# Kernel tuning notes

Hardware: AMD Instinct MI355X
Metric: run time of the kernel (lower is better)

Reference implementation:

```python
import jax, jax.numpy as jnp
import numpy as np
from jax import lax

EPS = 1e-8

def squash(x, axis=-1):
    # s = (|x|^2 / (1+|x|^2)) * x / |x|, norm over `axis`
    sq = jnp.sum(x * x, axis=axis, keepdims=True)
    return (sq / (1.0 + sq)) * x / jnp.sqrt(sq + EPS)

def _conv(x, w, b, stride):
    y = lax.conv_general_dilated(x, w, window_strides=(stride, stride), padding='VALID',
                                 dimension_numbers=('NCHW', 'OIHW', 'NCHW'))
    return y + b[None, :, None, None]

def setup_inputs() -> dict:
    key = jax.random.key(0)
    ks = jax.random.split(key, 12)
    B = 256
    return {
        'x': jax.random.uniform(ks[0], (B, 1, 28, 28), jnp.float32),
        'conv1_w': jax.random.normal(ks[1], (256, 1, 9, 9), jnp.float32) * 0.1,
        'conv1_b': jax.random.normal(ks[2], (256,), jnp.float32) * 0.01,
        'conv2_w': jax.random.normal(ks[3], (256, 256, 9, 9), jnp.float32) * 0.02,
        'conv2_b': jax.random.normal(ks[4], (256,), jnp.float32) * 0.01,
        'W': jax.random.normal(ks[5], (10, 1152, 8, 16), jnp.float32) * 0.05,
        'dec_w1': jax.random.normal(ks[6], (160, 512), jnp.float32) * 0.05,
        'dec_b1': jnp.zeros((512,), jnp.float32),
        'dec_w2': jax.random.normal(ks[7], (512, 1024), jnp.float32) * 0.04,
        'dec_b2': jnp.zeros((1024,), jnp.float32),
        'dec_w3': jax.random.normal(ks[8], (1024, 784), jnp.float32) * 0.03,
        'dec_b3': jnp.zeros((784,), jnp.float32),
    }

def reference(x, conv1_w, conv1_b, conv2_w, conv2_b, W, dec_w1, dec_b1, dec_w2, dec_b2, dec_w3, dec_b3):
    B = x.shape[0]
    h = jax.nn.relu(_conv(x, conv1_w, conv1_b, 1))          # [B,256,20,20]
    h = jax.nn.relu(_conv(h, conv2_w, conv2_b, 2))          # [B,256,6,6]
    u = squash(h.reshape(B, 1152, 8))                       # [B,1152,8]
    # u_hat[b,c,n,f] = sum_d u[b,n,d] * W[c,n,d,f]
    u_hat = jnp.einsum('bnd,cndf->bcnf', u, W)              # [B,10,1152,16]
    # dynamic routing, 3 iterations; softmax over the 1152 input-capsule axis
    # (faithful to original: softmax dim=2, b constant along the 16 axis)
    b_logits = jnp.zeros((B, 10, 1152), u_hat.dtype)
    v = None
    for i in range(3):
        c = jax.nn.softmax(b_logits, axis=2)                # [B,10,1152]
        s = jnp.einsum('bcn,bcnf->bcf', c, u_hat)           # [B,10,16]
        v = squash(s)
        if i != 2:
            b_logits = b_logits + jnp.einsum('bcf,bcnf->bcn', v, u_hat)
    class_probs = jnp.sqrt(jnp.sum(v * v, axis=-1) + EPS)   # [B,10]
    idx = jnp.argmax(class_probs, axis=-1)
    mask = jax.nn.one_hot(idx, 10, dtype=v.dtype)           # [B,10]
    r = (v * mask[:, :, None]).reshape(B, 160)
    r = jax.nn.relu(r @ dec_w1 + dec_b1)
    r = jax.nn.relu(r @ dec_w2 + dec_b2)
    recons = jax.nn.sigmoid(r @ dec_w3 + dec_b3)            # [B,784]
    return (class_probs, recons)
```

## Files before the change

kernel.cpp:

```cpp
#include <hip/hip_runtime.h>
#include <hip/hip_bf16.h>
#include <math.h>

typedef _Float16 f16;
typedef f16 f16x8 __attribute__((ext_vector_type(8)));
typedef f16 f16x4 __attribute__((ext_vector_type(4)));
typedef float f32x16 __attribute__((ext_vector_type(16)));


__global__ __launch_bounds__(256) void conv1_kernel(
    const float* __restrict__ x, const float* __restrict__ w,
    const float* __restrict__ bias, f16* __restrict__ outh,
    float* __restrict__ outf, int mode)
{
    const int b = blockIdx.y;
    const int cg = blockIdx.x;
    const int t = threadIdx.x;

    __shared__ float xs[784];
    __shared__ float wt[81 * 16];
    __shared__ float bs[16];

    for (int i = t; i < 784; i += 256) xs[i] = x[b * 784 + i];
    for (int i = t; i < 1296; i += 256) {
        int k = i >> 4, cc = i & 15;
        wt[i] = w[(cg * 16 + cc) * 81 + k];
    }
    if (t < 16) bs[t] = bias[cg * 16 + t];
    __syncthreads();

    if (t >= 200) return;
    const int pos = t * 2;
    const int oy = pos / 20, ox = pos % 20;
    float4 A0[4], A1[4];
    #pragma unroll
    for (int g = 0; g < 4; ++g) { A0[g] = make_float4(0,0,0,0); A1[g] = make_float4(0,0,0,0); }

    for (int ky = 0; ky < 9; ++ky) {
        const float* xr = &xs[(oy + ky) * 28 + ox];
        #pragma unroll
        for (int kx = 0; kx < 9; ++kx) {
            float x0 = xr[kx], x1 = xr[kx + 1];
            const float4* wp = (const float4*)&wt[(ky * 9 + kx) << 4];
            #pragma unroll
            for (int g = 0; g < 4; ++g) {
                float4 wv = wp[g];
                A0[g].x = fmaf(x0, wv.x, A0[g].x); A0[g].y = fmaf(x0, wv.y, A0[g].y);
                A0[g].z = fmaf(x0, wv.z, A0[g].z); A0[g].w = fmaf(x0, wv.w, A0[g].w);
                A1[g].x = fmaf(x1, wv.x, A1[g].x); A1[g].y = fmaf(x1, wv.y, A1[g].y);
                A1[g].z = fmaf(x1, wv.z, A1[g].z); A1[g].w = fmaf(x1, wv.w, A1[g].w);
            }
        }
    }

    float va[16], vb[16];
    #pragma unroll
    for (int g = 0; g < 4; ++g) {
        va[g*4+0] = fmaxf(A0[g].x + bs[g*4+0], 0.f);
        va[g*4+1] = fmaxf(A0[g].y + bs[g*4+1], 0.f);
        va[g*4+2] = fmaxf(A0[g].z + bs[g*4+2], 0.f);
        va[g*4+3] = fmaxf(A0[g].w + bs[g*4+3], 0.f);
        vb[g*4+0] = fmaxf(A1[g].x + bs[g*4+0], 0.f);
        vb[g*4+1] = fmaxf(A1[g].y + bs[g*4+1], 0.f);
        vb[g*4+2] = fmaxf(A1[g].z + bs[g*4+2], 0.f);
        vb[g*4+3] = fmaxf(A1[g].w + bs[g*4+3], 0.f);
    }

    if (mode == 0) {
        size_t base0 = ((size_t)b * 400 + pos) * 256 + cg * 16;
        f16x8 H;
        #pragma unroll
        for (int q = 0; q < 8; ++q) H[q] = (f16)va[q];
        *(f16x8*)(outh + base0) = H;
        #pragma unroll
        for (int q = 0; q < 8; ++q) H[q] = (f16)va[8+q];
        *(f16x8*)(outh + base0 + 8) = H;
        size_t base1 = base0 + 256;
        #pragma unroll
        for (int q = 0; q < 8; ++q) H[q] = (f16)vb[q];
        *(f16x8*)(outh + base1) = H;
        #pragma unroll
        for (int q = 0; q < 8; ++q) H[q] = (f16)vb[8+q];
        *(f16x8*)(outh + base1 + 8) = H;
    } else {
        #pragma unroll
        for (int q = 0; q < 16; ++q) {
            size_t base = (size_t)(b * 256 + cg * 16 + q) * 400 + pos;
            outf[base] = va[q]; outf[base + 1] = vb[q];
        }
    }
}

__global__ __launch_bounds__(256) void wprep_kernel(
    const float* __restrict__ w, f16* __restrict__ Wf)
{
    const int co = blockIdx.x, t = threadIdx.x;
    __shared__ float wl[20736];
    for (int i = t; i < 20736; i += 256) wl[i] = w[(size_t)co * 20736 + i];
    __syncthreads();
    for (int tap = 0; tap < 81; ++tap) {
        size_t o = ((size_t)tap * 256 + co) * 256 + t;
        Wf[o] = (f16)wl[t * 81 + tap];
    }
}

__global__ __launch_bounds__(256) void wprep2_kernel(
    const float* __restrict__ W, f16* __restrict__ Wr)
{
    const int i = blockIdx.x * 256 + threadIdx.x;
    Wr[i] = (f16)W[i];
}

struct C2R { f16x8 a0, a1, b0, b1, b2, b3; };

#define C2_LOADSET(R, gstep) do { \
    const int tap_ = (gstep) >> 3; \
    const int kc_ = ((gstep) & 7) << 5; \
    const int ky_ = tap_ / 9, kx_ = tap_ - ky_ * 9; \
    const int ao_ = (ky_ * 20 + kx_) * 256 + kc_; \
    const int bo_ = tap_ * 65536 + kc_; \
    R.a0 = *(const f16x8*)(A + paRow + ao_ + sl0 * 8); \
    R.a1 = *(const f16x8*)(A + paRow + ao_ + sl1 * 8); \
    R.b0 = *(const f16x8*)(B + pbRow + bo_); \
    R.b1 = *(const f16x8*)(B + pbRow + bo_ + 8); \
    R.b2 = *(const f16x8*)(B + pbRow + bo_ + 16); \
    R.b3 = *(const f16x8*)(B + pbRow + bo_ + 24); \
} while (0)

#define C2_STORESET(BB, R) do { \
    *(f16x8*)((char*)sA[BB] + wbA0) = R.a0; \
    *(f16x8*)((char*)sA[BB] + wbA1) = R.a1; \
    *(f16x8*)((char*)sB[BB] + wbB)          = R.b0; \
    *(f16x8*)((char*)sB[BB] + wbB + 4096)   = R.b1; \
    *(f16x8*)((char*)sB[BB] + wbB + 8192)   = R.b2; \
    *(f16x8*)((char*)sB[BB] + wbB + 12288)  = R.b3; \
} while (0)

#define C2_COMPUTE(BB) do { \
    _Pragma("unroll") \
    for (int h = 0; h < 2; ++h) { \
        f16x8 a0 = *(const f16x8*)((char*)sA[BB] + offA[h]); \
        f16x8 a1 = *(const f16x8*)((char*)sA[BB] + offA[h] + 512); \
        f16x8 b0 = *(const f16x8*)((char*)sB[BB] + offB[h]); \
        f16x8 b1 = *(const f16x8*)((char*)sB[BB] + offB[h] + 512); \
        f16x8 b2 = *(const f16x8*)((char*)sB[BB] + offB[h] + 1024); \
        f16x8 b3 = *(const f16x8*)((char*)sB[BB] + offB[h] + 1536); \
        acc00 = __builtin_amdgcn_mfma_f32_32x32x16_f16(a0, b0, acc00, 0, 0, 0); \
        acc01 = __builtin_amdgcn_mfma_f32_32x32x16_f16(a0, b1, acc01, 0, 0, 0); \
        acc02 = __builtin_amdgcn_mfma_f32_32x32x16_f16(a0, b2, acc02, 0, 0, 0); \
        acc03 = __builtin_amdgcn_mfma_f32_32x32x16_f16(a0, b3, acc03, 0, 0, 0); \
        acc10 = __builtin_amdgcn_mfma_f32_32x32x16_f16(a1, b0, acc10, 0, 0, 0); \
        acc11 = __builtin_amdgcn_mfma_f32_32x32x16_f16(a1, b1, acc11, 0, 0, 0); \
        acc12 = __builtin_amdgcn_mfma_f32_32x32x16_f16(a1, b2, acc12, 0, 0, 0); \
        acc13 = __builtin_amdgcn_mfma_f32_32x32x16_f16(a1, b3, acc13, 0, 0, 0); \
    } \
} while (0)

#define C2_BAR() do { \
    asm volatile("s_waitcnt lgkmcnt(0)" ::: "memory"); \
    __builtin_amdgcn_s_barrier(); \
    asm volatile("" ::: "memory"); \
} while (0)

__global__ __launch_bounds__(256, 2) void conv2_f16(
    const f16* __restrict__ A, const f16* __restrict__ B,
    float* __restrict__ partial, int nslice, int spk, int nwg)
{
    const int cpx = nwg >> 3;
    const int wg = (blockIdx.x & 7) * cpx + (blockIdx.x >> 3);
    const int mblk = wg / nslice;
    const int kslice = wg % nslice;

    const int t = threadIdx.x;
    const int lane = t & 63, wv = t >> 6;
    const int wm = wv >> 1, wn = wv & 1;

    __shared__ f16 sA[2][4096], sB[2][8192];

    const int strow = t >> 1;
    const int sl0 = (t & 1) * 2;
    const int sl1 = sl0 + 1;
    const int m0 = mblk * 128 + strow;
    const int b0_ = m0 / 36, s0_ = m0 % 36;
    const int paRow = b0_ * 102400 + ((s0_ / 6) * 40 + (s0_ % 6) * 2) * 256;
    const int pbRow = t * 256;

    const int wbA0 = sl0 * 2048 + strow * 16;
    const int wbA1 = sl1 * 2048 + strow * 16;
    const int wbB  = t * 16;

    const int kh = lane >> 5;
    const int rArow = wm * 64 + (lane & 31);
    const int rBrow = wn * 128 + (lane & 31);
    int offA[2], offB[2];
    #pragma unroll
    for (int h = 0; h < 2; ++h) {
        offA[h] = ((h * 2 + kh) << 11) + rArow * 16;
        offB[h] = ((h * 2 + kh) << 12) + rBrow * 16;
    }

    f32x16 acc00 = {}, acc01 = {}, acc02 = {}, acc03 = {};
    f32x16 acc10 = {}, acc11 = {}, acc12 = {}, acc13 = {};

    const int g0 = kslice * spk;
    C2R r0s, r1s;
    C2_LOADSET(r0s, g0);
    C2_LOADSET(r1s, g0 + 1);

    for (int s = 0; s < spk; s += 2) {
        C2_STORESET(0, r0s);
        C2_BAR();
        if (s + 2 < spk) C2_LOADSET(r0s, g0 + s + 2);
        C2_COMPUTE(0);

        C2_STORESET(1, r1s);
        C2_BAR();
        if (s + 3 < spk) C2_LOADSET(r1s, g0 + s + 3);
        C2_COMPUTE(1);
    }

    float* pp = partial + (size_t)kslice * 2359296;
    const int colb = wn * 128 + (lane & 31);
    const int rowb = mblk * 128 + wm * 64 + 4 * (lane >> 5);
    #pragma unroll
    for (int a = 0; a < 2; ++a) {
        #pragma unroll
        for (int nf = 0; nf < 4; ++nf) {
            const f32x16 v = (a == 0)
                ? (nf == 0 ? acc00 : nf == 1 ? acc01 : nf == 2 ? acc02 : acc03)
                : (nf == 0 ? acc10 : nf == 1 ? acc11 : nf == 2 ? acc12 : acc13);
            const int col = colb + nf * 32;
            const int rb = rowb + a * 32;
            #pragma unroll
            for (int r = 0; r < 16; ++r) {
                int row = rb + (r & 3) + 8 * (r >> 2);
                pp[(size_t)row * 256 + col] = v[r];
            }
        }
    }
}

__global__ __launch_bounds__(256) void reduce_kernel(
    const float* __restrict__ partial, const float* __restrict__ bias,
    float* __restrict__ u, int ks)
{
    const int b = blockIdx.x, t = threadIdx.x;
    __shared__ float ld[36 * 260];
    const int cog = t & 63;
    const int srow = t >> 6;
    const float4 bv = *(const float4*)(bias + cog * 4);
    #pragma unroll
    for (int q = 0; q < 9; ++q) {
        const int s = srow + q * 4;
        const size_t idx = ((size_t)(b * 36 + s)) * 256 + cog * 4;
        float4 a = bv;
        for (int k = 0; k < ks; ++k) {
            float4 p = *(const float4*)(partial + (size_t)k * 2359296 + idx);
            a.x += p.x; a.y += p.y; a.z += p.z; a.w += p.w;
        }
        a.x = fmaxf(a.x, 0.f); a.y = fmaxf(a.y, 0.f);
        a.z = fmaxf(a.z, 0.f); a.w = fmaxf(a.w, 0.f);
        *(float4*)&ld[s * 260 + cog * 4] = a;
    }
    __syncthreads();
    for (int n = t; n < 1152; n += 256) {
        const int f0 = n * 8;
        float vals[8]; float sq = 0.f;
        int co = f0 / 36;
        int s = f0 - co * 36;
        #pragma unroll
        for (int d = 0; d < 8; ++d) {
            float v = ld[s * 260 + co];
            vals[d] = v; sq += v * v;
            if (++s == 36) { s = 0; ++co; }
        }
        float scale = (sq / (1.f + sq)) / sqrtf(sq + 1e-8f);
        #pragma unroll
        for (int d = 0; d < 8; ++d) u[(size_t)b * 9216 + f0 + d] = vals[d] * scale;
    }
}

#define C2_CHUNK 2
__global__ __launch_bounds__(384) void conv2_kernel(
    const float* __restrict__ in, const float* __restrict__ w,
    const float* __restrict__ bias, float* __restrict__ out)
{
    const int bg = blockIdx.y;
    const int ct = blockIdx.x;
    const int t = threadIdx.x;

    __shared__ float wl[C2_CHUNK][81][64];
    __shared__ float il[C2_CHUNK][4][20][24];

    const int cg = t & 15;
    const int slot = t >> 4;
    const int bb = slot / 6;
    const int oy = slot % 6;

    float4 acc[6];
    #pragma unroll
    for (int i = 0; i < 6; ++i) acc[i] = make_float4(0,0,0,0);

    for (int cc0 = 0; cc0 < 256; cc0 += C2_CHUNK) {
        for (int idx = t; idx < C2_CHUNK * 5184; idx += 384) {
            int ci = idx / 5184;
            int r = idx - ci * 5184;
            int kk = r >> 6;
            int co = r & 63;
            wl[ci][kk][co] = w[(size_t)(ct * 64 + co) * 20736 + (cc0 + ci) * 81 + kk];
        }
        for (int idx = t; idx < C2_CHUNK * 1600; idx += 384) {
            int ci = idx / 1600;
            int r = idx - ci * 1600;
            int bb2 = r / 400;
            int p = r - bb2 * 400;
            int y = p / 20;
            int xx = p - y * 20;
            il[ci][bb2][y][(xx & 1) * 12 + (xx >> 1)] =
                in[(size_t)((bg * 4 + bb2) * 256 + cc0 + ci) * 400 + p];
        }
        __syncthreads();

        #pragma unroll
        for (int ci = 0; ci < C2_CHUNK; ++ci) {
            for (int ky = 0; ky < 9; ++ky) {
                const int y = oy * 2 + ky;
                const float4* rowp = (const float4*)&il[ci][bb][y][0];
                float a[24];
                #pragma unroll
                for (int q = 0; q < 6; ++q) *(((float4*)a) + q) = rowp[q];
                #pragma unroll
                for (int kx = 0; kx < 9; ++kx) {
                    const int k = ky * 9 + kx;
                    float4 wv = *(const float4*)&wl[ci][k][cg * 4];
                    const int base = (kx & 1) ? (12 + (kx >> 1)) : (kx >> 1);
                    #pragma unroll
                    for (int ox = 0; ox < 6; ++ox) {
                        float av = a[base + ox];
                        acc[ox].x = fmaf(av, wv.x, acc[ox].x);
                        acc[ox].y = fmaf(av, wv.y, acc[ox].y);
                        acc[ox].z = fmaf(av, wv.z, acc[ox].z);
                        acc[ox].w = fmaf(av, wv.w, acc[ox].w);
                    }
                }
            }
        }
        __syncthreads();
    }

    const int b = bg * 4 + bb;
    const int c0 = ct * 64 + cg * 4;
    float4 bv = *(const float4*)&bias[c0];
    #pragma unroll
    for (int ox = 0; ox < 6; ++ox) {
        int sdx = oy * 6 + ox;
        size_t ob = (size_t)b * 9216 + sdx;
        out[ob + (size_t)(c0 + 0) * 36] = fmaxf(acc[ox].x + bv.x, 0.f);
        out[ob + (size_t)(c0 + 1) * 36] = fmaxf(acc[ox].y + bv.y, 0.f);
        out[ob + (size_t)(c0 + 2) * 36] = fmaxf(acc[ox].z + bv.z, 0.f);
        out[ob + (size_t)(c0 + 3) * 36] = fmaxf(acc[ox].w + bv.w, 0.f);
    }
}

__global__ __launch_bounds__(256) void squash_kernel(float* __restrict__ h)
{
    const int cap = blockIdx.x * 256 + threadIdx.x;
    float4* p = (float4*)(h + (size_t)cap * 8);
    float4 v0 = p[0], v1 = p[1];
    float sq = v0.x*v0.x + v0.y*v0.y + v0.z*v0.z + v0.w*v0.w
             + v1.x*v1.x + v1.y*v1.y + v1.z*v1.z + v1.w*v1.w;
    float scale = (sq / (1.f + sq)) / sqrtf(sq + 1e-8f);
    v0.x *= scale; v0.y *= scale; v0.z *= scale; v0.w *= scale;
    v1.x *= scale; v1.y *= scale; v1.z *= scale; v1.w *= scale;
    p[0] = v0; p[1] = v1;
}

__global__ __launch_bounds__(256) void routing_kernel(
    const float* __restrict__ u, const f16* __restrict__ Wr,
    float* __restrict__ cp_out, float* __restrict__ vbuf)
{
    const int wg = ((blockIdx.x & 7) * 320) + (blockIdx.x >> 3);
    const int c = wg >> 8;
    const int b = wg & 255;
    const int t = threadIdx.x;
    const int lane = t & 63, wid = t >> 6;

    __shared__ float uh[1152 * 16];
    __shared__ float cl[1152];
    __shared__ float red[256];
    __shared__ float rtmp[8];
    __shared__ float vv[16];

    {
        const int fg = t & 3, ng = t >> 2;
        const f16* Wc = Wr + (size_t)c * 147456;
        const float* ub = u + (size_t)b * 9216;
        for (int j = 0; j < 18; ++j) {
            int n = ng + (j << 6);
            const f16* wn = Wc + n * 128 + fg * 4;
            float4 u0 = *(const float4*)(ub + n * 8);
            float4 u1 = *(const float4*)(ub + n * 8 + 4);
            float ud[8] = {u0.x, u0.y, u0.z, u0.w, u1.x, u1.y, u1.z, u1.w};
            float ax = 0.f, ay = 0.f, az = 0.f, aw = 0.f;
            #pragma unroll
            for (int d = 0; d < 8; ++d) {
                f16x4 w4 = *(const f16x4*)(wn + (d << 4));
                ax = fmaf(ud[d], (float)w4[0], ax);
                ay = fmaf(ud[d], (float)w4[1], ay);
                az = fmaf(ud[d], (float)w4[2], az);
                aw = fmaf(ud[d], (float)w4[3], aw);
            }
            *(float4*)&uh[(n << 4) + (fg << 2)] = make_float4(ax, ay, az, aw);
        }
    }
    __syncthreads();

    float blr[5] = {0.f, 0.f, 0.f, 0.f, 0.f};
    const int nown = (t < 128) ? 5 : 4;

    for (int it = 0; it < 3; ++it) {
        float m = -1e30f;
        #pragma unroll
        for (int k = 0; k < 5; ++k) if (k < nown) m = fmaxf(m, blr[k]);
        #pragma unroll
        for (int o = 32; o > 0; o >>= 1) m = fmaxf(m, __shfl_xor(m, o));
        if (lane == 0) rtmp[wid] = m;
        __syncthreads();
        m = fmaxf(fmaxf(rtmp[0], rtmp[1]), fmaxf(rtmp[2], rtmp[3]));

        float sum = 0.f;
        #pragma unroll
        for (int k = 0; k < 5; ++k) if (k < nown) {
            float e = __expf(blr[k] - m);
            cl[t + (k << 8)] = e;
            sum += e;
        }
        #pragma unroll
        for (int o = 32; o > 0; o >>= 1) sum += __shfl_xor(sum, o);
        if (lane == 0) rtmp[4 + wid] = sum;
        __syncthreads();
        float inv = 1.f / (rtmp[4] + rtmp[5] + rtmp[6] + rtmp[7]);

        const int f = t & 15, g = t >> 4;
        float sacc = 0.f;
        for (int n = g; n < 1152; n += 16)
            sacc = fmaf(cl[n], uh[(n << 4) + f], sacc);
        red[(g << 4) + f] = sacc;
        __syncthreads();
        if (t < 16) {
            float sv = 0.f;
            #pragma unroll
            for (int gg = 0; gg < 16; ++gg) sv += red[(gg << 4) + t];
            sv *= inv;
            float sq = sv * sv;
            #pragma unroll
            for (int o = 8; o > 0; o >>= 1) sq += __shfl_xor(sq, o);
            float scale = (sq / (1.f + sq)) / sqrtf(sq + 1e-8f);
            vv[t] = sv * scale;
        }
        __syncthreads();

        if (it < 2) {
            #pragma unroll
            for (int k = 0; k < 5; ++k) if (k < nown) {
                const int n = t + (k << 8);
                const float4* up = (const float4*)&uh[n << 4];
                float4 q0 = up[0], q1 = up[1], q2 = up[2], q3 = up[3];
                blr[k] +=
                    q0.x*vv[0]  + q0.y*vv[1]  + q0.z*vv[2]  + q0.w*vv[3] +
                    q1.x*vv[4]  + q1.y*vv[5]  + q1.z*vv[6]  + q1.w*vv[7] +
                    q2.x*vv[8]  + q2.y*vv[9]  + q2.z*vv[10] + q2.w*vv[11] +
                    q3.x*vv[12] + q3.y*vv[13] + q3.z*vv[14] + q3.w*vv[15];
            }
        }
    }

    if (t < 16) {
        float v_ = vv[t];
        float s2 = v_ * v_;
        #pragma unroll
        for (int o = 8; o > 0; o >>= 1) s2 += __shfl_xor(s2, o);
        if (t == 0) cp_out[b * 10 + c] = sqrtf(s2 + 1e-8f);
        vbuf[((b * 10 + c) << 4) + t] = v_;
    }
}

__global__ __launch_bounds__(256) void dec1_kernel(
    const float* __restrict__ cp, const float* __restrict__ vbuf,
    const float* __restrict__ W1, const float* __restrict__ B1,
    float* __restrict__ h1)
{
    const int b = blockIdx.x, t = threadIdx.x;
    __shared__ float r16[16];

    float best = cp[b * 10];
    int idx = 0;
    #pragma unroll
    for (int cc = 1; cc < 10; ++cc) {
        float p = cp[b * 10 + cc];
        if (p > best) { best = p; idx = cc; }
    }
    if (t < 16) r16[t] = vbuf[(b * 10 + idx) * 16 + t];
    __syncthreads();

    float a0 = B1[t], a1 = B1[t + 256];
    const float* w = W1 + (size_t)idx * 16 * 512 + t;
    #pragma unroll
    for (int k = 0; k < 16; ++k) {
        float rv = r16[k];
        a0 = fmaf(rv, w[k * 512], a0);
        a1 = fmaf(rv, w[k * 512 + 256], a1);
    }
    h1[(size_t)b * 512 + t] = fmaxf(a0, 0.f);
    h1[(size_t)b * 512 + t + 256] = fmaxf(a1, 0.f);
}

__global__ __launch_bounds__(256) void dec2_kernel(
    const float* __restrict__ h1, const float* __restrict__ W2,
    const float* __restrict__ B2, float* __restrict__ h2)
{
    const int ot = blockIdx.x, bt = blockIdx.y, t = threadIdx.x;
    const int bb = bt * 16 + (t >> 4);
    const int o = ot * 128 + (t & 15) * 8;

    float acc[8];
    float4 bv0 = *(const float4*)(B2 + o);
    float4 bv1 = *(const float4*)(B2 + o + 4);
    acc[0]=bv0.x; acc[1]=bv0.y; acc[2]=bv0.z; acc[3]=bv0.w;
    acc[4]=bv1.x; acc[5]=bv1.y; acc[6]=bv1.z; acc[7]=bv1.w;

    const float* hr = h1 + (size_t)bb * 512;
    #pragma unroll 4
    for (int k = 0; k < 512; ++k) {
        float hv = hr[k];
        float4 w0 = *(const float4*)(W2 + (size_t)k * 1024 + o);
        float4 w1 = *(const float4*)(W2 + (size_t)k * 1024 + o + 4);
        acc[0] = fmaf(hv, w0.x, acc[0]); acc[1] = fmaf(hv, w0.y, acc[1]);
        acc[2] = fmaf(hv, w0.z, acc[2]); acc[3] = fmaf(hv, w0.w, acc[3]);
        acc[4] = fmaf(hv, w1.x, acc[4]); acc[5] = fmaf(hv, w1.y, acc[5]);
        acc[6] = fmaf(hv, w1.z, acc[6]); acc[7] = fmaf(hv, w1.w, acc[7]);
    }
    float* hw = h2 + (size_t)bb * 1024 + o;
    #pragma unroll
    for (int q = 0; q < 8; ++q) hw[q] = fmaxf(acc[q], 0.f);
}

__global__ __launch_bounds__(256) void dec3_kernel(
    const float* __restrict__ h2, const float* __restrict__ W3,
    const float* __restrict__ B3, float* __restrict__ out)
{
    const int ot = blockIdx.x, bt = blockIdx.y, t = threadIdx.x;
    const int bb = bt * 16 + (t >> 4);
    const int o = ot * 64 + (t & 15) * 4;
    if (o >= 784) return;

    float4 bv = *(const float4*)(B3 + o);
    float acc[4] = {bv.x, bv.y, bv.z, bv.w};

    const float* hr = h2 + (size_t)bb * 1024;
    #pragma unroll 4
    for (int k = 0; k < 1024; ++k) {
        float hv = hr[k];
        float4 w0 = *(const float4*)(W3 + (size_t)k * 784 + o);
        acc[0] = fmaf(hv, w0.x, acc[0]); acc[1] = fmaf(hv, w0.y, acc[1]);
        acc[2] = fmaf(hv, w0.z, acc[2]); acc[3] = fmaf(hv, w0.w, acc[3]);
    }
    float* ow = out + (size_t)bb * 784 + o;
    #pragma unroll
    for (int q = 0; q < 4; ++q) ow[q] = 1.f / (1.f + expf(-acc[q]));
}

extern "C" void kernel_launch(void* const* d_in, const int* in_sizes, int n_in,
                              void* d_out, int out_size, void* d_ws, size_t ws_size,
                              hipStream_t stream) {
    const float* x   = (const float*)d_in[0];
    const float* w1  = (const float*)d_in[1];
    const float* b1  = (const float*)d_in[2];
    const float* w2  = (const float*)d_in[3];
    const float* b2  = (const float*)d_in[4];
    const float* W   = (const float*)d_in[5];
    const float* dw1 = (const float*)d_in[6];
    const float* db1 = (const float*)d_in[7];
    const float* dw2 = (const float*)d_in[8];
    const float* db2 = (const float*)d_in[9];
    const float* dw3 = (const float*)d_in[10];
    const float* db3 = (const float*)d_in[11];

    float* ws   = (float*)d_ws;
    float* outp = (float*)d_out;

    const size_t avail = ws_size / 4;
    int ks = 0;
    if      (avail >= 16498688ull + 6*2359296ull + 40960ull) ks = 6;
    else if (avail >= 16498688ull + 4*2359296ull + 40960ull) ks = 4;
    else if (avail >= 16498688ull + 2*2359296ull + 40960ull) ks = 2;
    else if (avail >= 16498688ull + 1*2359296ull + 40960ull) ks = 1;

    if (ks > 0) {
        f16* Af = (f16*)ws;
        f16* Wf = (f16*)(ws + 13107200);
        f16* Wr = (f16*)(ws + 15761408);
        float* partial = ws + 16498688;
        float* vbuf = ws + 16498688 + (size_t)ks * 2359296;
        float* u  = ws;
        float* h1 = ws + 13107200;
        float* h2 = ws + 13238272;

        const int nwg = 72 * ks;
        conv1_kernel<<<dim3(16, 256), 256, 0, stream>>>(x, w1, b1, Af, nullptr, 0);
        wprep_kernel<<<256, 256, 0, stream>>>(w2, Wf);
        wprep2_kernel<<<5760, 256, 0, stream>>>(W, Wr);
        conv2_f16<<<nwg, 256, 0, stream>>>(Af, Wf, partial, ks, 648 / ks, nwg);
        reduce_kernel<<<256, 256, 0, stream>>>(partial, b2, u, ks);
        routing_kernel<<<2560, 256, 0, stream>>>(u, Wr, outp, vbuf);
        dec1_kernel<<<256, 256, 0, stream>>>(outp, vbuf, dw1, db1, h1);
        dec2_kernel<<<dim3(8, 16), 256, 0, stream>>>(h1, dw2, db2, h2);
        dec3_kernel<<<dim3(13, 16), 256, 0, stream>>>(h2, dw3, db3, outp + 2560);
    } else {
        float* c1   = ws;
        float* c2   = c1 + 26214400;
        float* vbuf = c2 + 2359296;
        float* h1   = vbuf + 40960;
        float* h2   = h1 + 131072;
        f16* Wr     = (f16*)(h2 + 262144);
        conv1_kernel<<<dim3(16, 256), 256, 0, stream>>>(x, w1, b1, nullptr, c1, 1);
        wprep2_kernel<<<5760, 256, 0, stream>>>(W, Wr);
        conv2_kernel<<<dim3(4, 64), 384, 0, stream>>>(c1, w2, b2, c2);
        squash_kernel<<<1152, 256, 0, stream>>>(c2);
        routing_kernel<<<2560, 256, 0, stream>>>(c2, Wr, outp, vbuf);
        dec1_kernel<<<256, 256, 0, stream>>>(outp, vbuf, dw1, db1, h1);
        dec2_kernel<<<dim3(8, 16), 256, 0, stream>>>(h1, dw2, db2, h2);
        dec3_kernel<<<dim3(13, 16), 256, 0, stream>>>(h2, dw3, db3, outp + 2560);
    }
}
```

Before: 540.1 us.

## Store conv2 split-K partials as f16 transposed and raise split count

The conv2 split-K partial sums are now stored as f16 in a channel-major transposed layout, which halves partial-buffer traffic and lets the reduce kernel read contiguous f16x4 runs per channel. The split count rises to as many as 12 slices, adding more workgroups for better GPU fill, and the launch-bounds occupancy hint goes from 2 to 3. An odd-spk tail is also handled. Rounding partials to f16 before the sum costs some accuracy, and more slices add reduce work.

Result: slower. 917.5 us (+69.9%).

```diff
diff --git a/kernel.cpp b/kernel.cpp
--- a/kernel.cpp
+++ b/kernel.cpp
@@ -162,9 +162,9 @@
     asm volatile("" ::: "memory"); \
 } while (0)
 
-__global__ __launch_bounds__(256, 2) void conv2_f16(
+__global__ __launch_bounds__(256, 3) void conv2_f16(
     const f16* __restrict__ A, const f16* __restrict__ B,
-    float* __restrict__ partial, int nslice, int spk, int nwg)
+    f16* __restrict__ partial, int nslice, int spk, int nwg)
 {
     const int cpx = nwg >> 3;
     const int wg = (blockIdx.x & 7) * cpx + (blockIdx.x >> 3);
@@ -205,9 +205,10 @@
     const int g0 = kslice * spk;
     C2R r0s, r1s;
     C2_LOADSET(r0s, g0);
-    C2_LOADSET(r1s, g0 + 1);
-
-    for (int s = 0; s < spk; s += 2) {
+    if (spk > 1) C2_LOADSET(r1s, g0 + 1);
+
+    int s = 0;
+    for (; s + 1 < spk; s += 2) {
         C2_STORESET(0, r0s);
         C2_BAR();
         if (s + 2 < spk) C2_LOADSET(r0s, g0 + s + 2);
@@ -218,8 +219,13 @@
         if (s + 3 < spk) C2_LOADSET(r1s, g0 + s + 3);
         C2_COMPUTE(1);
     }
-
-    float* pp = partial + (size_t)kslice * 2359296;
+    if (s < spk) {
+        C2_STORESET(0, r0s);
+        C2_BAR();
+        C2_COMPUTE(0);
+    }
+
+    f16* pp = partial + (size_t)kslice * 2359296;
     const int colb = wn * 128 + (lane & 31);
     const int rowb = mblk * 128 + wm * 64 + 4 * (lane >> 5);
     #pragma unroll
@@ -232,47 +238,53 @@
             const int col = colb + nf * 32;
             const int rb = rowb + a * 32;
             #pragma unroll
-            for (int r = 0; r < 16; ++r) {
-                int row = rb + (r & 3) + 8 * (r >> 2);
-                pp[(size_t)row * 256 + col] = v[r];
+            for (int q = 0; q < 4; ++q) {
+                f16x4 o;
+                #pragma unroll
+                for (int j = 0; j < 4; ++j) o[j] = (f16)v[q * 4 + j];
+                *(f16x4*)(pp + (size_t)col * 9216 + rb + 8 * q) = o;
             }
         }
     }
 }
 
 __global__ __launch_bounds__(256) void reduce_kernel(
-    const float* __restrict__ partial, const float* __restrict__ bias,
+    const f16* __restrict__ partial, const float* __restrict__ bias,
     float* __restrict__ u, int ks)
 {
     const int b = blockIdx.x, t = threadIdx.x;
     __shared__ float ld[36 * 260];
-    const int cog = t & 63;
-    const int srow = t >> 6;
-    const float4 bv = *(const float4*)(bias + cog * 4);
-    #pragma unroll
-    for (int q = 0; q < 9; ++q) {
-        const int s = srow + q * 4;
-        const size_t idx = ((size_t)(b * 36 + s)) * 256 + cog * 4;
-        float4 a = bv;
-        for (int k = 0; k < ks; ++k) {
-            float4 p = *(const float4*)(partial + (size_t)k * 2359296 + idx);
-            a.x += p.x; a.y += p.y; a.z += p.z; a.w += p.w;
-        }
-        a.x = fmaxf(a.x, 0.f); a.y = fmaxf(a.y, 0.f);
-        a.z = fmaxf(a.z, 0.f); a.w = fmaxf(a.w, 0.f);
-        *(float4*)&ld[s * 260 + cog * 4] = a;
-    }
+
+    float acc[36];
+    const float bv = bias[t];
+    #pragma unroll
+    for (int si = 0; si < 36; ++si) acc[si] = bv;
+
+    for (int k = 0; k < ks; ++k) {
+        const f16* pp = partial + (size_t)k * 2359296 + (size_t)t * 9216 + b * 36;
+        #pragma unroll
+        for (int q = 0; q < 9; ++q) {
+            f16x4 p4 = *(const f16x4*)(pp + q * 4);
+            acc[q*4+0] += (float)p4[0];
+            acc[q*4+1] += (float)p4[1];
+            acc[q*4+2] += (float)p4[2];
+            acc[q*4+3] += (float)p4[3];
+        }
+    }
+    #pragma unroll
+    for (int si = 0; si < 36; ++si) ld[si * 260 + t] = fmaxf(acc[si], 0.f);
     __syncthreads();
+
     for (int n = t; n < 1152; n += 256) {
         const int f0 = n * 8;
         float vals[8]; float sq = 0.f;
         int co = f0 / 36;
-        int s = f0 - co * 36;
+        int si = f0 - co * 36;
         #pragma unroll
         for (int d = 0; d < 8; ++d) {
-            float v = ld[s * 260 + co];
+            float v = ld[si * 260 + co];
             vals[d] = v; sq += v * v;
-            if (++s == 36) { s = 0; ++co; }
+            if (++si == 36) { si = 0; ++co; }
         }
         float scale = (sq / (1.f + sq)) / sqrtf(sq + 1e-8f);
         #pragma unroll
@@ -591,17 +603,19 @@
 
     const size_t avail = ws_size / 4;
     int ks = 0;
-    if      (avail >= 16498688ull + 6*2359296ull + 40960ull) ks = 6;
-    else if (avail >= 16498688ull + 4*2359296ull + 40960ull) ks = 4;
-    else if (avail >= 16498688ull + 2*2359296ull + 40960ull) ks = 2;
-    else if (avail >= 16498688ull + 1*2359296ull + 40960ull) ks = 1;
+    if      (avail >= 16498688ull + 12*1179648ull + 40960ull) ks = 12;
+    else if (avail >= 16498688ull +  8*1179648ull + 40960ull) ks = 8;
+    else if (avail >= 16498688ull +  6*1179648ull + 40960ull) ks = 6;
+    else if (avail >= 16498688ull +  4*1179648ull + 40960ull) ks = 4;
+    else if (avail >= 16498688ull +  2*1179648ull + 40960ull) ks = 2;
+    else if (avail >= 16498688ull +  1*1179648ull + 40960ull) ks = 1;
 
     if (ks > 0) {
         f16* Af = (f16*)ws;
         f16* Wf = (f16*)(ws + 13107200);
         f16* Wr = (f16*)(ws + 15761408);
-        float* partial = ws + 16498688;
-        float* vbuf = ws + 16498688 + (size_t)ks * 2359296;
+        f16* partial = (f16*)(ws + 16498688);
+        float* vbuf = ws + 16498688 + (size_t)ks * 1179648;
         float* u  = ws;
         float* h1 = ws + 13107200;
         float* h2 = ws + 13238272;
```
